# Kernel tuning notes

Measured on AMD Instinct MI355X. Metric: run time of the kernel, lower is better.

Reference implementation:

```python
import jax, jax.numpy as jnp
import numpy as np

B, T, D_IN, D_OUT = 8, 4096, 512, 512
STYLE, RANK, ALPHA = 256, 8, 1.0
NUM_LORA = (D_IN + D_OUT) * RANK


def setup_inputs() -> dict:
    key = jax.random.key(0)
    ks = jax.random.split(key, 8)
    s = 0.02
    return {
        "x": jax.random.normal(ks[0], (B, T, D_IN), jnp.float32),
        "style_emb": jax.random.normal(ks[1], (B, STYLE), jnp.float32),
        "w_base": jax.random.normal(ks[2], (D_OUT, D_IN), jnp.float32) * s,
        "b_base": jax.random.normal(ks[3], (D_OUT,), jnp.float32) * s,
        "w_h1": jax.random.normal(ks[4], (STYLE, STYLE), jnp.float32) * s,
        "b_h1": jax.random.normal(ks[5], (STYLE,), jnp.float32) * s,
        "w_h2": jax.random.normal(ks[6], (NUM_LORA, STYLE), jnp.float32) * s,
        "b_h2": jax.random.normal(ks[7], (NUM_LORA,), jnp.float32) * s,
    }


def reference(x, style_emb, w_base, b_base, w_h1, b_h1, w_h2, b_h2):
    # Base linear: [B,T,D_out]
    base_out = jnp.einsum("btd,od->bto", x, w_base) + b_base
    # Hypernet: Linear -> SiLU -> Linear producing per-sample LoRA params
    h = jax.nn.silu(style_emb @ w_h1.T + b_h1)          # [B, STYLE]
    raw = h @ w_h2.T + b_h2                             # [B, NUM_LORA]
    split = D_IN * RANK
    mat_a = raw[:, :split].reshape(B, RANK, D_IN)       # [B, r, D_in]
    mat_b = raw[:, split:].reshape(B, D_OUT, RANK)      # [B, D_out, r]
    # Low-rank path: x @ A^T @ B^T  (never materialize [B,D_out,D_in])
    down = jnp.einsum("btd,brd->btr", x, mat_a)         # [B, T, r]
    lora = jnp.einsum("btr,bor->bto", down, mat_b)      # [B, T, D_out]
    return base_out + ALPHA * lora
```

## Files before the change

kernel.cpp:

```cpp
#include <hip/hip_runtime.h>
#include <hip/hip_fp16.h>
#include <stdint.h>


#define NB 8
#define NT 4096
#define DIN 512
#define DOUT 512
#define NSTYLE 256
#define RANK 8
#define NLORA ((DIN + DOUT) * RANK)

typedef _Float16 f16x8 __attribute__((ext_vector_type(8)));
typedef float f32x4 __attribute__((ext_vector_type(4)));

__global__ void k_hyper1(const float* __restrict__ style,
                         const float* __restrict__ w_h1,
                         const float* __restrict__ b_h1,
                         float* __restrict__ h) {
  const int b = blockIdx.x;
  const int j = threadIdx.x;
  __shared__ float s[NSTYLE];
  s[j] = style[b * NSTYLE + j];
  __syncthreads();
  const float4* wrow = (const float4*)(w_h1 + (size_t)j * NSTYLE);
  float acc = b_h1[j];
#pragma unroll 8
  for (int k = 0; k < NSTYLE / 4; ++k) {
    float4 w4 = wrow[k];
    acc += s[4 * k + 0] * w4.x + s[4 * k + 1] * w4.y + s[4 * k + 2] * w4.z +
           s[4 * k + 3] * w4.w;
  }
  h[b * NSTYLE + j] = acc / (1.f + expf(-acc));
}

__global__ __launch_bounds__(256) void k_hyper2(const float* __restrict__ h,
                                                const float* __restrict__ w_h2,
                                                const float* __restrict__ b_h2,
                                                float* __restrict__ raw) {
  __shared__ float hs[NB * NSTYLE];
  const int t = threadIdx.x;
#pragma unroll
  for (int i = 0; i < NB * NSTYLE / 256; ++i) hs[i * 256 + t] = h[i * 256 + t];
  __syncthreads();
  const int w = t >> 6, lane = t & 63;
  const int n = blockIdx.x * 4 + w;
  float4 w4 = *(const float4*)(w_h2 + (size_t)n * NSTYLE + lane * 4);
  float acc[NB];
#pragma unroll
  for (int b = 0; b < NB; ++b) {
    float4 hb = *(const float4*)(&hs[b * NSTYLE + lane * 4]);
    acc[b] = hb.x * w4.x + hb.y * w4.y + hb.z * w4.z + hb.w * w4.w;
#pragma unroll
    for (int m = 32; m > 0; m >>= 1) acc[b] += __shfl_xor(acc[b], m);
  }
  if (lane == 0) {
    const float bb = b_h2[n];
#pragma unroll
    for (int b = 0; b < NB; ++b) raw[(size_t)b * NLORA + n] = acc[b] + bb;
  }
}

__global__ void k_weff(const float* __restrict__ raw,
                       const float* __restrict__ w_base,
                       _Float16* __restrict__ Whf) {
  const int cg = blockIdx.x;
  const int b = blockIdx.y;
  const int t = threadIdx.x;
  __shared__ float Als[RANK * DIN];
  __shared__ float Wbs[16 * 516];
  __shared__ float Bls[16][RANK];
  const float* rb = raw + (size_t)b * NLORA;
#pragma unroll
  for (int i = 0; i < 4; ++i)
    *(float4*)(&Als[(i * 256 + t) * 4]) = *(const float4*)(&rb[(i * 256 + t) * 4]);
#pragma unroll
  for (int i = 0; i < 8; ++i) {
    int fi = i * 256 + t;
    int oo = fi >> 7, d4 = fi & 127;
    float4 v = *(const float4*)(&w_base[((size_t)(cg * 16 + oo)) * DIN + d4 * 4]);
    *(float4*)(&Wbs[oo * 516 + d4 * 4]) = v;
  }
  if (t < 16 * RANK) {
    int oo = t >> 3, r = t & 7;
    Bls[oo][r] = rb[DIN * RANK + (cg * 16 + oo) * RANK + r];
  }
  __syncthreads();
  const int lane = t & 63;
  const int oo = lane & 15;
  const int koff = ((lane >> 4) & 3) * 8;
  float br[RANK];
#pragma unroll
  for (int r = 0; r < RANK; ++r) br[r] = Bls[oo][r];
  _Float16* dst = Whf + (size_t)b * (DOUT * DIN) + cg * 8192;
#pragma unroll
  for (int i = 0; i < 4; ++i) {
    const int q = i * 256 + t;
    const int kkg = q >> 6;
    const int kb = kkg * 32 + koff;
    f16x8 v;
#pragma unroll
    for (int j = 0; j < 8; ++j) {
      float a = Wbs[oo * 516 + kb + j];
#pragma unroll
      for (int r = 0; r < RANK; ++r) a += br[r] * Als[r * DIN + kb + j];
      v[j] = (_Float16)a;
    }
    *(f16x8*)(dst + (size_t)q * 8) = v;
  }
}

#define BM 32
#define BK 64

__global__ __launch_bounds__(256, 3) void k_gemm(
    const float* __restrict__ x, const _Float16* __restrict__ Whf,
    const float* __restrict__ b_base, float* __restrict__ out) {
  const int id = blockIdx.x;
  const int b = id & 7;
  const int mt = id >> 3;
  const int t = threadIdx.x;
  const int lane = t & 63;
  const int w = t >> 6;
  const int l16 = lane & 15, lq = lane >> 4;

  __shared__ _Float16 Xs[2][BM * BK];

  const float* xb = x + ((size_t)b * NT + (size_t)mt * BM) * DIN;
  const _Float16* wb = Whf + (size_t)b * (DOUT * DIN) + (size_t)(w * 8) * 8192 +
                       (size_t)lane * 8;

  f32x4 acc[2][8];
#pragma unroll
  for (int m = 0; m < 2; ++m)
#pragma unroll
    for (int n = 0; n < 8; ++n)
#pragma unroll
      for (int j = 0; j < 4; ++j) acc[m][n][j] = 0.f;

  const int srow = t >> 3, sc = t & 7;
  const float* xsrc = xb + (size_t)srow * DIN + sc * 8;
  const int swz_w = (srow * 128 + sc * 16) ^ ((srow & 7) << 4);

  {
    float4 f0 = *(const float4*)(xsrc + 0);
    float4 f1 = *(const float4*)(xsrc + 4);
    f16x8 hh;
    hh[0] = (_Float16)f0.x; hh[1] = (_Float16)f0.y;
    hh[2] = (_Float16)f0.z; hh[3] = (_Float16)f0.w;
    hh[4] = (_Float16)f1.x; hh[5] = (_Float16)f1.y;
    hh[6] = (_Float16)f1.z; hh[7] = (_Float16)f1.w;
    *(f16x8*)((char*)&Xs[0][0] + swz_w) = hh;
  }
  __syncthreads();

  for (int step = 0; step < DIN / BK; ++step) {
    const int cur = step & 1;
    float4 f0p, f1p;
    if (step < DIN / BK - 1) {
      f0p = *(const float4*)(xsrc + (step + 1) * BK + 0);
      f1p = *(const float4*)(xsrc + (step + 1) * BK + 4);
    }
#pragma unroll
    for (int kk = 0; kk < 2; ++kk) {
      const int kkg = step * 2 + kk;
      f16x8 af[2], bf[8];
#pragma unroll
      for (int m = 0; m < 2; ++m) {
        const int row = m * 16 + l16;
        const int byte = (row * 128 + (kk * 4 + lq) * 16) ^ ((row & 7) << 4);
        af[m] = *(const f16x8*)((const char*)&Xs[cur][0] + byte);
      }
#pragma unroll
      for (int n = 0; n < 8; ++n)
        bf[n] = *(const f16x8*)(wb + (size_t)n * 8192 + (size_t)kkg * 512);
#pragma unroll
      for (int m = 0; m < 2; ++m)
#pragma unroll
        for (int n = 0; n < 8; ++n)
          acc[m][n] = __builtin_amdgcn_mfma_f32_16x16x32_f16(af[m], bf[n],
                                                             acc[m][n], 0, 0, 0);
    }
    if (step < DIN / BK - 1) {
      f16x8 hh;
      hh[0] = (_Float16)f0p.x; hh[1] = (_Float16)f0p.y;
      hh[2] = (_Float16)f0p.z; hh[3] = (_Float16)f0p.w;
      hh[4] = (_Float16)f1p.x; hh[5] = (_Float16)f1p.y;
      hh[6] = (_Float16)f1p.z; hh[7] = (_Float16)f1p.w;
      *(f16x8*)((char*)&Xs[cur ^ 1][0] + swz_w) = hh;
    }
    __syncthreads();
  }

  float bv[8];
#pragma unroll
  for (int n = 0; n < 8; ++n) bv[n] = b_base[w * 128 + n * 16 + l16];

#pragma unroll
  for (int m = 0; m < 2; ++m) {
#pragma unroll
    for (int j = 0; j < 4; ++j) {
      const int r = mt * BM + m * 16 + lq * 4 + j;
      float* orow = out + ((size_t)b * NT + r) * DOUT;
#pragma unroll
      for (int n = 0; n < 8; ++n)
        orow[w * 128 + n * 16 + l16] = acc[m][n][j] + bv[n];
    }
  }
}

extern "C" void kernel_launch(void* const* d_in, const int* in_sizes, int n_in,
                              void* d_out, int out_size, void* d_ws,
                              size_t ws_size, hipStream_t stream) {
  const float* x = (const float*)d_in[0];
  const float* style = (const float*)d_in[1];
  const float* w_base = (const float*)d_in[2];
  const float* b_base = (const float*)d_in[3];
  const float* w_h1 = (const float*)d_in[4];
  const float* b_h1 = (const float*)d_in[5];
  const float* w_h2 = (const float*)d_in[6];
  const float* b_h2 = (const float*)d_in[7];
  float* out = (float*)d_out;

  char* ws = (char*)d_ws;
  float* h = (float*)ws;
  float* raw = (float*)(ws + 8192);
  _Float16* Whf = (_Float16*)(ws + 8192 + 262144);

  k_hyper1<<<NB, NSTYLE, 0, stream>>>(style, w_h1, b_h1, h);
  k_hyper2<<<NLORA / 4, 256, 0, stream>>>(h, w_h2, b_h2, raw);
  k_weff<<<dim3(DOUT / 16, NB), 256, 0, stream>>>(raw, w_base, Whf);
  k_gemm<<<(NT / BM) * NB, 256, 0, stream>>>(x, Whf, b_base, out);
}
```

Before: 184.1 us.

## Retile GEMM to 128x128 blocks with LDS-staged weights via global_load_lds

Changes the main GEMM from 32-row blocks covering the full output width to 128x128 output tiles, with four waves arranged 2x2. Weight fragments are now staged into shared memory with direct global-to-LDS loads instead of being read per wave from global memory. The goal is more reuse of each X and W load and fewer global weight reads. In exchange, the old double-buffered X prefetch is dropped, so loads are no longer overlapped with compute. The launch-bounds occupancy hint is also removed, and X is now read four times, once per column tile.

```diff
diff --git a/kernel.cpp b/kernel.cpp
--- a/kernel.cpp
+++ b/kernel.cpp
@@ -110,101 +110,102 @@
   }
 }
 
-#define BM 32
+#define BM 128
+#define BN 128
 #define BK 64
 
-__global__ __launch_bounds__(256, 3) void k_gemm(
+__global__ __launch_bounds__(256) void k_gemm(
     const float* __restrict__ x, const _Float16* __restrict__ Whf,
     const float* __restrict__ b_base, float* __restrict__ out) {
   const int id = blockIdx.x;
   const int b = id & 7;
-  const int mt = id >> 3;
+  const int nt = (id >> 3) & 3;
+  const int mt = id >> 5;
   const int t = threadIdx.x;
   const int lane = t & 63;
-  const int w = t >> 6;
+  const int wave = t >> 6;
+  const int wr = wave >> 1, wc = wave & 1;
   const int l16 = lane & 15, lq = lane >> 4;
 
-  __shared__ _Float16 Xs[2][BM * BK];
+  __shared__ _Float16 Xs[BM * BK];
+  __shared__ _Float16 Ws[BN * BK];
 
   const float* xb = x + ((size_t)b * NT + (size_t)mt * BM) * DIN;
-  const _Float16* wb = Whf + (size_t)b * (DOUT * DIN) + (size_t)(w * 8) * 8192 +
-                       (size_t)lane * 8;
-
-  f32x4 acc[2][8];
-#pragma unroll
-  for (int m = 0; m < 2; ++m)
-#pragma unroll
-    for (int n = 0; n < 8; ++n)
+  const _Float16* wbt = Whf + (size_t)b * (DOUT * DIN) + (size_t)(nt * 8) * 8192;
+
+  f32x4 acc[4][4];
+#pragma unroll
+  for (int m = 0; m < 4; ++m)
+#pragma unroll
+    for (int n = 0; n < 4; ++n)
 #pragma unroll
       for (int j = 0; j < 4; ++j) acc[m][n][j] = 0.f;
 
-  const int srow = t >> 3, sc = t & 7;
-  const float* xsrc = xb + (size_t)srow * DIN + sc * 8;
-  const int swz_w = (srow * 128 + sc * 16) ^ ((srow & 7) << 4);
-
-  {
-    float4 f0 = *(const float4*)(xsrc + 0);
-    float4 f1 = *(const float4*)(xsrc + 4);
-    f16x8 hh;
-    hh[0] = (_Float16)f0.x; hh[1] = (_Float16)f0.y;
-    hh[2] = (_Float16)f0.z; hh[3] = (_Float16)f0.w;
-    hh[4] = (_Float16)f1.x; hh[5] = (_Float16)f1.y;
-    hh[6] = (_Float16)f1.z; hh[7] = (_Float16)f1.w;
-    *(f16x8*)((char*)&Xs[0][0] + swz_w) = hh;
-  }
-  __syncthreads();
-
   for (int step = 0; step < DIN / BK; ++step) {
-    const int cur = step & 1;
-    float4 f0p, f1p;
-    if (step < DIN / BK - 1) {
-      f0p = *(const float4*)(xsrc + (step + 1) * BK + 0);
-      f1p = *(const float4*)(xsrc + (step + 1) * BK + 4);
-    }
+    __syncthreads();
+#pragma unroll
+    for (int i = 0; i < 4; ++i) {
+      const int p = i * 256 + t;
+      const int row = p >> 3, o8 = p & 7;
+      const float* src = xb + (size_t)row * DIN + step * BK + o8 * 8;
+      float4 f0 = *(const float4*)(src);
+      float4 f1 = *(const float4*)(src + 4);
+      f16x8 hh;
+      hh[0] = (_Float16)f0.x; hh[1] = (_Float16)f0.y;
+      hh[2] = (_Float16)f0.z; hh[3] = (_Float16)f0.w;
+      hh[4] = (_Float16)f1.x; hh[5] = (_Float16)f1.y;
+      hh[6] = (_Float16)f1.z; hh[7] = (_Float16)f1.w;
+      const int byte = (row * 128 + o8 * 16) ^ ((row & 7) << 4);
+      *(f16x8*)((char*)Xs + byte) = hh;
+    }
+#pragma unroll
+    for (int i = 0; i < 4; ++i) {
+      const int c = i * 256 + t;
+      const int cgr = c >> 7, kkr = (c >> 6) & 1, e = c & 63;
+      const _Float16* g = wbt + (size_t)cgr * 8192 + (size_t)(step * 2 + kkr) * 512 + e * 8;
+      __builtin_amdgcn_global_load_lds(
+          (const __attribute__((address_space(1))) void*)g,
+          (__attribute__((address_space(3))) void*)((char*)Ws +
+                                                    (i * 256 + wave * 64) * 16),
+          16, 0, 0);
+    }
+    __syncthreads();
 #pragma unroll
     for (int kk = 0; kk < 2; ++kk) {
-      const int kkg = step * 2 + kk;
-      f16x8 af[2], bf[8];
-#pragma unroll
-      for (int m = 0; m < 2; ++m) {
-        const int row = m * 16 + l16;
+      f16x8 af[4], bf[4];
+#pragma unroll
+      for (int m = 0; m < 4; ++m) {
+        const int row = wr * 64 + m * 16 + l16;
         const int byte = (row * 128 + (kk * 4 + lq) * 16) ^ ((row & 7) << 4);
-        af[m] = *(const f16x8*)((const char*)&Xs[cur][0] + byte);
+        af[m] = *(const f16x8*)((const char*)Xs + byte);
       }
 #pragma unroll
-      for (int n = 0; n < 8; ++n)
-        bf[n] = *(const f16x8*)(wb + (size_t)n * 8192 + (size_t)kkg * 512);
-#pragma unroll
-      for (int m = 0; m < 2; ++m)
-#pragma unroll
-        for (int n = 0; n < 8; ++n)
+      for (int n = 0; n < 4; ++n)
+        bf[n] = *(const f16x8*)((const char*)Ws +
+                                (((wc * 4 + n) * 2 + kk) * 1024 + lane * 16));
+#pragma unroll
+      for (int m = 0; m < 4; ++m)
+#pragma unroll
+        for (int n = 0; n < 4; ++n)
           acc[m][n] = __builtin_amdgcn_mfma_f32_16x16x32_f16(af[m], bf[n],
                                                              acc[m][n], 0, 0, 0);
     }
-    if (step < DIN / BK - 1) {
-      f16x8 hh;
-      hh[0] = (_Float16)f0p.x; hh[1] = (_Float16)f0p.y;
-      hh[2] = (_Float16)f0p.z; hh[3] = (_Float16)f0p.w;
-      hh[4] = (_Float16)f1p.x; hh[5] = (_Float16)f1p.y;
-      hh[6] = (_Float16)f1p.z; hh[7] = (_Float16)f1p.w;
-      *(f16x8*)((char*)&Xs[cur ^ 1][0] + swz_w) = hh;
-    }
-    __syncthreads();
-  }
-
-  float bv[8];
-#pragma unroll
-  for (int n = 0; n < 8; ++n) bv[n] = b_base[w * 128 + n * 16 + l16];
-
-#pragma unroll
-  for (int m = 0; m < 2; ++m) {
+  }
+
+  float bv[4];
+#pragma unroll
+  for (int n = 0; n < 4; ++n)
+    bv[n] = b_base[nt * BN + wc * 64 + n * 16 + l16];
+
+#pragma unroll
+  for (int m = 0; m < 4; ++m) {
 #pragma unroll
     for (int j = 0; j < 4; ++j) {
-      const int r = mt * BM + m * 16 + lq * 4 + j;
-      float* orow = out + ((size_t)b * NT + r) * DOUT;
-#pragma unroll
-      for (int n = 0; n < 8; ++n)
-        orow[w * 128 + n * 16 + l16] = acc[m][n][j] + bv[n];
+      const int r = mt * BM + wr * 64 + m * 16 + lq * 4 + j;
+      float* orow = out + ((size_t)b * NT + r) * DOUT + nt * BN;
+#pragma unroll
+      for (int n = 0; n < 4; ++n)
+        orow[wc * 64 + n * 16 + l16] = acc[m][n][j] + bv[n];
     }
   }
 }
@@ -230,5 +231,5 @@
   k_hyper1<<<NB, NSTYLE, 0, stream>>>(style, w_h1, b_h1, h);
   k_hyper2<<<NLORA / 4, 256, 0, stream>>>(h, w_h2, b_h2, raw);
   k_weff<<<dim3(DOUT / 16, NB), 256, 0, stream>>>(raw, w_base, Whf);
-  k_gemm<<<(NT / BM) * NB, 256, 0, stream>>>(x, Whf, b_base, out);
-}
+  k_gemm<<<(NT / BM) * (DOUT / BN) * NB, 256, 0, stream>>>(x, Whf, b_base, out);
+}
```

Result: no change. 181.2 us (-1.6%).
